# Kernel tuning notes

Hardware: AMD Instinct MI355X
Metric: run time of the kernel (lower is better)

## Reference

```python
import jax, jax.numpy as jnp
import numpy as np

EMBED = 1024
HEADS = 16
HEAD_DIM = EMBED // HEADS
SCALING = HEAD_DIM ** -0.5
R = 16
LORA_SCALE = 32.0 / R  # alpha / r
NEG = jnp.finfo(jnp.float32).min


def lora_linear(x, W, A, B):
    # y = x @ W.T + (x @ A.T) @ B.T * scale   (LinearLora, bias=False)
    return x @ W.T + ((x @ A.T) @ B.T) * LORA_SCALE


def setup_inputs() -> dict:
    key = jax.random.key(0)
    ks = jax.random.split(key, 14)
    B, T, D = 1, 4096, EMBED
    hidden_states = jax.random.normal(ks[0], (B, T, D), jnp.float32)
    # causal additive mask (bsz, 1, tgt, src): 0 on/below diag, dtype-min above
    i = jnp.arange(T)
    causal = jnp.where(i[:, None] >= i[None, :], 0.0, NEG).astype(jnp.float32)
    attention_mask = jnp.broadcast_to(causal, (B, 1, T, T))
    s = 0.02
    def w(k, shape):
        return jax.random.normal(k, shape, jnp.float32) * s
    return dict(
        hidden_states=hidden_states,
        attention_mask=attention_mask,
        Wq=w(ks[1], (D, D)), Wk=w(ks[2], (D, D)), Wv=w(ks[3], (D, D)), Wo=w(ks[4], (D, D)),
        Aq=w(ks[5], (R, D)), Bq=jnp.zeros((D, R), jnp.float32) + w(ks[6], (D, R)),
        Ak=w(ks[7], (R, D)), Bk=w(ks[8], (D, R)),
        Av=w(ks[9], (R, D)), Bv=w(ks[10], (D, R)),
        Ao=w(ks[11], (R, D)), Bo=w(ks[12], (D, R)),
    )


def reference(hidden_states, attention_mask, Wq, Wk, Wv, Wo,
              Aq, Bq, Ak, Bk, Av, Bv, Ao, Bo):
    bsz, tgt_len, _ = hidden_states.shape
    H, Hd = HEADS, HEAD_DIM

    q = lora_linear(hidden_states, Wq, Aq, Bq) * SCALING
    k = lora_linear(hidden_states, Wk, Ak, Bk)
    v = lora_linear(hidden_states, Wv, Av, Bv)

    # (b, t, H, Hd)
    q = q.reshape(bsz, tgt_len, H, Hd)
    k = k.reshape(bsz, tgt_len, H, Hd)
    v = v.reshape(bsz, tgt_len, H, Hd)

    # scores (b, H, t, s)
    attn = jnp.einsum('bthd,bshd->bhts', q, k)
    attn = attn + attention_mask
    attn = jnp.maximum(attn, NEG)
    attn = jax.nn.softmax(attn, axis=-1)  # dropout p=0 / eval mode

    out = jnp.einsum('bhts,bshd->bthd', attn, v)
    out = out.reshape(bsz, tgt_len, H * Hd)
    out = lora_linear(out, Wo, Ao, Bo)
    return out
```

## Files before the change

### kernel.cpp

```cpp
#include <hip/hip_runtime.h>
#include <cmath>
#include <cstdint>

typedef unsigned short u16;
typedef __attribute__((ext_vector_type(8))) __bf16 bf16x8;
typedef __attribute__((ext_vector_type(4))) __bf16 bf16x4;
typedef __attribute__((ext_vector_type(4))) short s16x4;
typedef __attribute__((ext_vector_type(4))) float f32x4;

__device__ __forceinline__ u16 f2bf(float f) {
    union { float f; unsigned u; } v; v.f = f;
    unsigned r = v.u + 0x7fffu + ((v.u >> 16) & 1u);
    return (u16)(r >> 16);
}

__device__ __forceinline__ void gload_lds(const u16* g, u16* l) {
    __builtin_amdgcn_global_load_lds((__attribute__((address_space(1))) void*)g,
                                     (__attribute__((address_space(3))) void*)l,
                                     16, 0, 0);
}

__device__ __forceinline__ f32x4 mfma16(s16x4 a, s16x4 b, f32x4 c) {
#if __has_builtin(__builtin_amdgcn_mfma_f32_16x16x16bf16_1k)
    return __builtin_amdgcn_mfma_f32_16x16x16bf16_1k(a, b, c, 0, 0, 0);
#else
    asm("v_mfma_f32_16x16x16_bf16 %0, %1, %2, %3"
        : "=v"(c) : "v"(a), "v"(b), "0"(c));
    return c;
#endif
}

__global__ __launch_bounds__(256) void prep_all(
        const float* __restrict__ X,
        const float* __restrict__ Wq, const float* __restrict__ Wk,
        const float* __restrict__ Wv, const float* __restrict__ Wo,
        const float* __restrict__ Aq, const float* __restrict__ Bq,
        const float* __restrict__ Ak, const float* __restrict__ Bk,
        const float* __restrict__ Av, const float* __restrict__ Bv,
        const float* __restrict__ Ao, const float* __restrict__ Bo,
        u16* __restrict__ Wqkv, u16* __restrict__ Wob, u16* __restrict__ Xb) {
    const int p = blockIdx.y;
    const int idx = blockIdx.x * 256 + threadIdx.x;
    if (p == 4) {
        float4 v = ((const float4*)X)[idx];
        ushort4 o;
        o.x = f2bf(v.x); o.y = f2bf(v.y); o.z = f2bf(v.z); o.w = f2bf(v.w);
        ((ushort4*)Xb)[idx] = o;
        return;
    }
    const int n = idx >> 10, d = idx & 1023;
    const float* W; const float* A; const float* B;
    switch (p) {
        case 0: W = Wq; A = Aq; B = Bq; break;
        case 1: W = Wk; A = Ak; B = Bk; break;
        case 2: W = Wv; A = Av; B = Bv; break;
        default: W = Wo; A = Ao; B = Bo; break;
    }
    float lora = 0.f;
#pragma unroll
    for (int r = 0; r < 16; r++) lora += B[n * 16 + r] * A[r * 1024 + d];
    float v = W[idx] + 2.0f * lora;
    if (p == 0) v *= 0.125f * 1.44269504088896340736f;
    if (p < 3) Wqkv[(size_t)p * 1048576 + idx] = f2bf(v);
    else       Wob[idx] = f2bf(v);
}

template <bool F32OUT>
__global__ __launch_bounds__(256, 3) void gemm_bt(const u16* __restrict__ A,
                                                  const u16* __restrict__ B,
                                                  void* __restrict__ C, int ldc) {
    __shared__ __align__(16) u16 As[128 * 64];
    __shared__ __align__(16) u16 Bs[128 * 64];
    const int tid = threadIdx.x;
    const int lane = tid & 63, wave = tid >> 6;
    const int quad = lane >> 4, l16 = lane & 15;
    const int wm = (wave >> 1) * 64, wn = (wave & 1) * 64;
    const size_t m0 = (size_t)blockIdx.y * 128, n0 = (size_t)blockIdx.x * 128;
    const u16* Ap = A + m0 * 1024;
    const u16* Bp = B + n0 * 1024;
    const int xsw = l16 & 7;
    f32x4 acc[4][4] = {};
    for (int k0 = 0; k0 < 1024; k0 += 64) {
#pragma unroll
        for (int hh = 0; hh < 4; hh++) {
            int c = tid + hh * 256;
            int row = c >> 3, cg = (c & 7) ^ (row & 7);
            gload_lds(Ap + (size_t)row * 1024 + k0 + cg * 8, As + c * 8);
            gload_lds(Bp + (size_t)row * 1024 + k0 + cg * 8, Bs + c * 8);
        }
        asm volatile("s_waitcnt vmcnt(0)" ::: "memory");
        __syncthreads();
#pragma unroll
        for (int kf = 0; kf < 2; kf++) {
            bf16x8 af[4], bfr[4];
#pragma unroll
            for (int i = 0; i < 4; i++) {
                af[i]  = *(const bf16x8*)(As + (wm + i * 16 + l16) * 64
                                             + ((kf * 4 + quad) ^ xsw) * 8);
                bfr[i] = *(const bf16x8*)(Bs + (wn + i * 16 + l16) * 64
                                             + ((kf * 4 + quad) ^ xsw) * 8);
            }
#pragma unroll
            for (int mi = 0; mi < 4; mi++)
#pragma unroll
                for (int ni = 0; ni < 4; ni++)
                    acc[mi][ni] = __builtin_amdgcn_mfma_f32_16x16x32_bf16(
                            af[mi], bfr[ni], acc[mi][ni], 0, 0, 0);
        }
        __syncthreads();
    }
#pragma unroll
    for (int mi = 0; mi < 4; mi++)
#pragma unroll
        for (int ni = 0; ni < 4; ni++)
#pragma unroll
            for (int r = 0; r < 4; r++) {
                size_t row = m0 + wm + mi * 16 + quad * 4 + r;
                size_t col = n0 + wn + ni * 16 + l16;
                if (F32OUT) ((float*)C)[row * ldc + col] = acc[mi][ni][r];
                else        ((u16*)C)[row * ldc + col] = f2bf(acc[mi][ni][r]);
            }
}

template <bool F32OUT>
__global__ __launch_bounds__(256, 3) void gemm_bt64(const u16* __restrict__ A,
                                                    const u16* __restrict__ B,
                                                    void* __restrict__ C, int ldc) {
    __shared__ __align__(16) u16 As[64 * 64];
    __shared__ __align__(16) u16 Bs[128 * 64];
    const int tid = threadIdx.x;
    const int lane = tid & 63, wave = tid >> 6;
    const int quad = lane >> 4, l16 = lane & 15;
    const int wm = (wave >> 1) * 32, wn = (wave & 1) * 64;
    const size_t m0 = (size_t)blockIdx.y * 64, n0 = (size_t)blockIdx.x * 128;
    const u16* Ap = A + m0 * 1024;
    const u16* Bp = B + n0 * 1024;
    const int xsw = l16 & 7;
    f32x4 acc[2][4] = {};
    for (int k0 = 0; k0 < 1024; k0 += 64) {
#pragma unroll
        for (int hh = 0; hh < 2; hh++) {
            int c = tid + hh * 256;
            int row = c >> 3, cg = (c & 7) ^ (row & 7);
            gload_lds(Ap + (size_t)row * 1024 + k0 + cg * 8, As + c * 8);
        }
#pragma unroll
        for (int hh = 0; hh < 4; hh++) {
            int c = tid + hh * 256;
            int row = c >> 3, cg = (c & 7) ^ (row & 7);
            gload_lds(Bp + (size_t)row * 1024 + k0 + cg * 8, Bs + c * 8);
        }
        asm volatile("s_waitcnt vmcnt(0)" ::: "memory");
        __syncthreads();
#pragma unroll
        for (int kf = 0; kf < 2; kf++) {
            bf16x8 af[2], bfr[4];
#pragma unroll
            for (int i = 0; i < 2; i++)
                af[i] = *(const bf16x8*)(As + (wm + i * 16 + l16) * 64
                                            + ((kf * 4 + quad) ^ xsw) * 8);
#pragma unroll
            for (int i = 0; i < 4; i++)
                bfr[i] = *(const bf16x8*)(Bs + (wn + i * 16 + l16) * 64
                                             + ((kf * 4 + quad) ^ xsw) * 8);
#pragma unroll
            for (int mi = 0; mi < 2; mi++)
#pragma unroll
                for (int ni = 0; ni < 4; ni++)
                    acc[mi][ni] = __builtin_amdgcn_mfma_f32_16x16x32_bf16(
                            af[mi], bfr[ni], acc[mi][ni], 0, 0, 0);
        }
        __syncthreads();
    }
#pragma unroll
    for (int mi = 0; mi < 2; mi++)
#pragma unroll
        for (int ni = 0; ni < 4; ni++)
#pragma unroll
            for (int r = 0; r < 4; r++) {
                size_t row = m0 + wm + mi * 16 + quad * 4 + r;
                size_t col = n0 + wn + ni * 16 + l16;
                if (F32OUT) ((float*)C)[row * ldc + col] = acc[mi][ni][r];
                else        ((u16*)C)[row * ldc + col] = f2bf(acc[mi][ni][r]);
            }
}

__global__ __launch_bounds__(256) void transpose_v(const u16* __restrict__ Y,
                                                   u16* __restrict__ Vt) {
    __shared__ u16 tile[64][68];
    const int dv0 = blockIdx.x * 64;
    const int t0  = blockIdx.y * 64;
    const int tid = threadIdx.x;
#pragma unroll
    for (int p = 0; p < 4; p++) {
        int pos = tid + p * 256;
        int row = pos >> 4;
        int c4  = (pos & 15) * 4;
        ushort4 v = *(const ushort4*)(Y + (size_t)(t0 + row) * 3072 + 2048 + dv0 + c4);
        tile[row][c4 + 0] = v.x; tile[row][c4 + 1] = v.y;
        tile[row][c4 + 2] = v.z; tile[row][c4 + 3] = v.w;
    }
    __syncthreads();
#pragma unroll
    for (int p = 0; p < 4; p++) {
        int pos = tid + p * 256;
        int orow = pos >> 4;
        int oc4  = (pos & 15) * 4;
        ushort4 o;
        o.x = tile[oc4 + 0][orow]; o.y = tile[oc4 + 1][orow];
        o.z = tile[oc4 + 2][orow]; o.w = tile[oc4 + 3][orow];
        *(ushort4*)(Vt + (size_t)(dv0 + orow) * 4096 + t0 + oc4) = o;
    }
}

__device__ const unsigned char SCHED[48] = {
    (1<<6)|31, (0<<6)|15, (1<<6)|30, (2<<6)|30, (2<<6)|29, (0<<6)|14, (2<<6)|28, (1<<6)|27,
    (2<<6)|27, (0<<6)|13, (2<<6)|26, (2<<6)|25, (0<<6)|12, (1<<6)|24, (2<<6)|24, (2<<6)|23,
    (2<<6)|31, (1<<6)|29, (1<<6)|28, (1<<6)|26, (1<<6)|25, (1<<6)|23, (1<<6)|22, (1<<6)|21,
    (1<<6)|20, (2<<6)|20, (1<<6)|19, (2<<6)|19, (2<<6)|21, (2<<6)|22, (0<<6)|10, (0<<6)|11,
    (0<<6)|0,  (0<<6)|1,  (0<<6)|2,  (0<<6)|3,  (0<<6)|4,  (0<<6)|5,  (0<<6)|6,  (0<<6)|7,
    (1<<6)|16, (2<<6)|16, (1<<6)|18, (0<<6)|9,  (1<<6)|17, (2<<6)|17, (2<<6)|18, (0<<6)|8
};

__global__ __launch_bounds__(256, 3) void flash_attn(
        const u16* __restrict__ Y,
        const u16* __restrict__ Vt,
        u16* __restrict__ O,
        float* __restrict__ OpA,
        float* __restrict__ OpB,
        float* __restrict__ lA,
        float* __restrict__ lB) {
    __shared__ __align__(16) u16 lds[24576];
    const int tid = threadIdx.x;
    const int wave = tid >> 6, lane = tid & 63;
    const int quad = lane >> 4, l16 = lane & 15;
    const int bid = blockIdx.x;
    const int g = bid >> 4, h = bid & 15;
    const int sc = SCHED[g];
    const int p = sc & 63, mode = sc >> 6;
    const int t0 = (mode == 2) ? p + 1 : 0;
    const int t1 = (mode == 1) ? p + 1 : 2 * p + 2;
    const int q0w = p * 128 + wave * 32;
    const u16* Kbase = Y + 1024 + h * 64;
    const u16* Vbase = Vt + (size_t)(h * 64) * 4096;
    const int xsw = l16 & 7;

#define STAGE(TT, BUF) do {                                                   \
        const int sss = (TT) * 64;                                            \
        u16* Kn_ = (BUF);                                                     \
        _Pragma("unroll")                                                     \
        for (int pp = 0; pp < 2; pp++) {                                      \
            int c = pp * 256 + tid;                                           \
            int row_ = c >> 3, cg_ = (c & 7) ^ (row_ & 7);                    \
            gload_lds(Kbase + (size_t)(sss + row_) * 3072 + cg_ * 8,          \
                      Kn_ + c * 8);                                           \
            gload_lds(Vbase + (size_t)row_ * 4096 + sss + cg_ * 8,            \
                      Kn_ + 4096 + c * 8);                                    \
        }                                                                     \
    } while (0)

    bf16x8 qf[2][2];
#pragma unroll
    for (int qh = 0; qh < 2; qh++)
#pragma unroll
        for (int kf = 0; kf < 2; kf++)
            qf[qh][kf] = *(const bf16x8*)(Y + (size_t)(q0w + qh * 16 + l16) * 3072
                                            + h * 64 + kf * 32 + quad * 8);

    f32x4 oaccT[2][4] = {};
    f32x4 lacc[2] = {};
    const s16x4 ones = { (short)0x3F80, (short)0x3F80,
                         (short)0x3F80, (short)0x3F80 };

    STAGE(t0, lds);
    if (t0 + 1 < t1) STAGE(t0 + 1, lds + 8192);

    int cur = 0;
    int nxt = 2;
#pragma unroll 1
    for (int t = t0; t < t1; t++) {
        const int s0 = t * 64;
        u16* Ks = lds + cur * 8192;
        u16* Vs = Ks + 4096;
        if (t + 1 < t1) asm volatile("s_waitcnt vmcnt(4)" ::: "memory");
        else            asm volatile("s_waitcnt vmcnt(0)" ::: "memory");
        __syncthreads();

        if (t + 2 < t1) STAGE(t + 2, lds + nxt * 8192);

        bf16x8 kfr[4][2];
#pragma unroll
        for (int ni = 0; ni < 4; ni++) {
            int row = ni * 16 + l16;
            kfr[ni][0] = *(const bf16x8*)(Ks + row * 64 + ((quad) ^ xsw) * 8);
            kfr[ni][1] = *(const bf16x8*)(Ks + row * 64 + ((4 + quad) ^ xsw) * 8);
        }
        s16x4 vfr[4][4];
#pragma unroll
        for (int nj = 0; nj < 4; nj++) {
            int row = nj * 16 + l16;
#pragma unroll
            for (int ni = 0; ni < 4; ni++) {
                int cc = ni * 2 + (quad >> 1);
                vfr[nj][ni] = *(const s16x4*)(Vs + row * 64 + (cc ^ xsw) * 8
                                                 + (quad & 1) * 4);
            }
        }

        const bool diag = (t >= 2 * p);
#pragma unroll
        for (int qh = 0; qh < 2; qh++) {
            f32x4 sacc[4] = {};
            __builtin_amdgcn_s_setprio(1);
#pragma unroll
            for (int ni = 0; ni < 4; ni++) {
                sacc[ni] = __builtin_amdgcn_mfma_f32_16x16x32_bf16(
                        kfr[ni][0], qf[qh][0], sacc[ni], 0, 0, 0);
                sacc[ni] = __builtin_amdgcn_mfma_f32_16x16x32_bf16(
                        kfr[ni][1], qf[qh][1], sacc[ni], 0, 0, 0);
            }
            __builtin_amdgcn_s_setprio(0);
            const int qg = q0w + qh * 16 + l16;
#pragma unroll
            for (int ni = 0; ni < 4; ni++) {
                if (diag) {
#pragma unroll
                    for (int r = 0; r < 4; r++) {
                        int sg = s0 + ni * 16 + quad * 4 + r;
                        if (sg > qg) sacc[ni][r] = -INFINITY;
                    }
                }
                f32x4 pe;
#pragma unroll
                for (int r = 0; r < 4; r++)
                    pe[r] = __builtin_amdgcn_exp2f(sacc[ni][r]);
                bf16x4 tt = { (__bf16)pe[0], (__bf16)pe[1],
                              (__bf16)pe[2], (__bf16)pe[3] };
                s16x4 pf = __builtin_bit_cast(s16x4, tt);
                __builtin_amdgcn_s_setprio(1);
                lacc[qh] = mfma16(ones, pf, lacc[qh]);
#pragma unroll
                for (int nj = 0; nj < 4; nj++)
                    oaccT[qh][nj] = mfma16(vfr[nj][ni], pf, oaccT[qh][nj]);
                __builtin_amdgcn_s_setprio(0);
            }
        }
        cur = (cur == 2) ? 0 : cur + 1;
        nxt = (nxt == 2) ? 0 : nxt + 1;
    }
#undef STAGE

    __syncthreads();
    if (mode == 0) {
        u16* scr = lds + wave * 1152;
#pragma unroll
        for (int qh = 0; qh < 2; qh++) {
            float inv = 1.0f / lacc[qh][0];
#pragma unroll
            for (int nj = 0; nj < 4; nj++) {
                bf16x4 t4 = { (__bf16)(oaccT[qh][nj][0] * inv),
                              (__bf16)(oaccT[qh][nj][1] * inv),
                              (__bf16)(oaccT[qh][nj][2] * inv),
                              (__bf16)(oaccT[qh][nj][3] * inv) };
                *(s16x4*)(scr + l16 * 72 + nj * 16 + quad * 4) =
                        __builtin_bit_cast(s16x4, t4);
            }
            asm volatile("s_waitcnt lgkmcnt(0)" ::: "memory");
#pragma unroll
            for (int pp = 0; pp < 2; pp++) {
                int row = pp * 8 + (lane >> 3);
                int seg = (lane & 7) * 8;
                bf16x8 d = *(const bf16x8*)(scr + row * 72 + seg);
                *(bf16x8*)(O + (size_t)(q0w + qh * 16 + row) * 1024 + h * 64 + seg) = d;
            }
            asm volatile("s_waitcnt lgkmcnt(0)" ::: "memory");
        }
    } else {
        float* Op = (mode == 1) ? OpA : OpB;
        float* lp = (mode == 1) ? lA : lB;
        float* scr = (float*)lds + wave * 1088;
#pragma unroll
        for (int qh = 0; qh < 2; qh++) {
#pragma unroll
            for (int nj = 0; nj < 4; nj++)
                *(f32x4*)(scr + l16 * 68 + nj * 16 + quad * 4) = oaccT[qh][nj];
            asm volatile("s_waitcnt lgkmcnt(0)" ::: "memory");
#pragma unroll
            for (int it = 0; it < 4; it++) {
                int row = (lane >> 4) + it * 4;
                int seg = (lane & 15) * 4;
                f32x4 d = *(const f32x4*)(scr + row * 68 + seg);
                *(f32x4*)(Op + (size_t)(q0w + qh * 16 + row - 2048) * 1024
                             + h * 64 + seg) = d;
            }
            if (lane < 16)
                lp[(size_t)(q0w + qh * 16 + lane - 2048) * 16 + h] = lacc[qh][0];
            asm volatile("s_waitcnt lgkmcnt(0)" ::: "memory");
        }
    }
}

__global__ __launch_bounds__(256) void combine_o(
        const float* __restrict__ OpA, const float* __restrict__ OpB,
        const float* __restrict__ lA, const float* __restrict__ lB,
        u16* __restrict__ O) {
    const int idx = blockIdx.x * 256 + threadIdx.x;
    const int r = idx >> 7;
    const int c8 = (idx & 127) * 8;
    const int h = c8 >> 6;
    const float inv = 1.0f / (lA[r * 16 + h] + lB[r * 16 + h]);
    const float* a = OpA + (size_t)r * 1024 + c8;
    const float* b = OpB + (size_t)r * 1024 + c8;
    float4 a0 = *(const float4*)a, a1 = *(const float4*)(a + 4);
    float4 b0 = *(const float4*)b, b1 = *(const float4*)(b + 4);
    ushort4 o0, o1;
    o0.x = f2bf((a0.x + b0.x) * inv); o0.y = f2bf((a0.y + b0.y) * inv);
    o0.z = f2bf((a0.z + b0.z) * inv); o0.w = f2bf((a0.w + b0.w) * inv);
    o1.x = f2bf((a1.x + b1.x) * inv); o1.y = f2bf((a1.y + b1.y) * inv);
    o1.z = f2bf((a1.z + b1.z) * inv); o1.w = f2bf((a1.w + b1.w) * inv);
    u16* op = O + (size_t)(2048 + r) * 1024 + c8;
    *(ushort4*)op = o0;
    *(ushort4*)(op + 4) = o1;
}


extern "C" void kernel_launch(void* const* d_in, const int* in_sizes, int n_in,
                              void* d_out, int out_size, void* d_ws, size_t ws_size,
                              hipStream_t stream) {
    const float* X  = (const float*)d_in[0];
    const float* Wq = (const float*)d_in[2];
    const float* Wk = (const float*)d_in[3];
    const float* Wv = (const float*)d_in[4];
    const float* Wo = (const float*)d_in[5];
    const float* Aq = (const float*)d_in[6];
    const float* Bq = (const float*)d_in[7];
    const float* Ak = (const float*)d_in[8];
    const float* Bk = (const float*)d_in[9];
    const float* Av = (const float*)d_in[10];
    const float* Bv = (const float*)d_in[11];
    const float* Ao = (const float*)d_in[12];
    const float* Bo = (const float*)d_in[13];

    char* ws = (char*)d_ws;
    u16*   Xb   = (u16*)(ws);
    float* OpA  = (float*)(ws);
    u16*   Wqkv = (u16*)(ws + (8u  << 20));
    float* OpB  = (float*)(ws + (8u  << 20));
    u16*   Y    = (u16*)(ws + (16u << 20));
    u16*   Vt   = (u16*)(ws + (40u << 20));
    u16*   Ob   = (u16*)(ws + (48u << 20));
    u16*   Wob  = (u16*)(ws + (56u << 20));
    float* lA   = (float*)(ws + (58u << 20));
    float* lB   = (float*)(ws + (58u << 20) + (128u << 10));

    prep_all<<<dim3(4096, 5), 256, 0, stream>>>(X, Wq, Wk, Wv, Wo, Aq, Bq, Ak, Bk,
                                                Av, Bv, Ao, Bo, Wqkv, Wob, Xb);
    gemm_bt<false><<<dim3(24, 32), 256, 0, stream>>>(Xb, Wqkv, Y, 3072);
    transpose_v<<<dim3(16, 64), 256, 0, stream>>>(Y, Vt);
    flash_attn<<<dim3(768), 256, 0, stream>>>(Y, Vt, Ob, OpA, OpB, lA, lB);
    combine_o<<<dim3(1024), 256, 0, stream>>>(OpA, OpB, lA, lB, Ob);
    gemm_bt64<true><<<dim3(8, 64), 256, 0, stream>>>(Ob, Wob, d_out, 1024);
}
```

Baseline: 255.9 us.

## Replace QKV GEMM with 256x192 double-buffered tile kernel using 512 threads

```diff
diff --git a/kernel.cpp b/kernel.cpp
--- a/kernel.cpp
+++ b/kernel.cpp
@@ -65,60 +65,98 @@
     else       Wob[idx] = f2bf(v);
 }
 
-template <bool F32OUT>
-__global__ __launch_bounds__(256, 3) void gemm_bt(const u16* __restrict__ A,
-                                                  const u16* __restrict__ B,
-                                                  void* __restrict__ C, int ldc) {
-    __shared__ __align__(16) u16 As[128 * 64];
-    __shared__ __align__(16) u16 Bs[128 * 64];
+__global__ __launch_bounds__(512, 2) void gemm_bt256(const u16* __restrict__ A,
+                                                     const u16* __restrict__ B,
+                                                     u16* __restrict__ C, int ldc) {
+    __shared__ __align__(16) u16 As[2][256 * 64];
+    __shared__ __align__(16) u16 Bs[2][192 * 64];
     const int tid = threadIdx.x;
-    const int lane = tid & 63, wave = tid >> 6;
+    const int lane = tid & 63;
+    const int wave = tid >> 6;
     const int quad = lane >> 4, l16 = lane & 15;
-    const int wm = (wave >> 1) * 64, wn = (wave & 1) * 64;
-    const size_t m0 = (size_t)blockIdx.y * 128, n0 = (size_t)blockIdx.x * 128;
+    const int wm = (wave >> 2) * 128;
+    const int wn = (wave & 3) * 48;
+    const size_t m0 = (size_t)blockIdx.y * 256, n0 = (size_t)blockIdx.x * 192;
     const u16* Ap = A + m0 * 1024;
     const u16* Bp = B + n0 * 1024;
     const int xsw = l16 & 7;
-    f32x4 acc[4][4] = {};
-    for (int k0 = 0; k0 < 1024; k0 += 64) {
-#pragma unroll
-        for (int hh = 0; hh < 4; hh++) {
-            int c = tid + hh * 256;
-            int row = c >> 3, cg = (c & 7) ^ (row & 7);
-            gload_lds(Ap + (size_t)row * 1024 + k0 + cg * 8, As + c * 8);
-            gload_lds(Bp + (size_t)row * 1024 + k0 + cg * 8, Bs + c * 8);
-        }
-        asm volatile("s_waitcnt vmcnt(0)" ::: "memory");
+
+#define STAGEA(T, BUF) do {                                                   \
+        _Pragma("unroll")                                                     \
+        for (int hh = 0; hh < 4; hh++) {                                      \
+            int c = tid + hh * 512;                                           \
+            int row_ = c >> 3, cg_ = (c & 7) ^ (row_ & 7);                    \
+            gload_lds(Ap + (size_t)row_ * 1024 + (T) * 64 + cg_ * 8,          \
+                      (BUF) + c * 8);                                         \
+        }                                                                     \
+    } while (0)
+#define STAGEB(T, BUF) do {                                                   \
+        _Pragma("unroll")                                                     \
+        for (int hh = 0; hh < 3; hh++) {                                      \
+            int c = tid + hh * 512;                                           \
+            int row_ = c >> 3, cg_ = (c & 7) ^ (row_ & 7);                    \
+            gload_lds(Bp + (size_t)row_ * 1024 + (T) * 64 + cg_ * 8,          \
+                      (BUF) + c * 8);                                         \
+        }                                                                     \
+    } while (0)
+
+    f32x4 acc[8][3] = {};
+
+    STAGEA(0, As[0]);
+    STAGEB(0, Bs[0]);
+    asm volatile("s_waitcnt vmcnt(0)" ::: "memory");
+    __syncthreads();
+
+#pragma unroll 1
+    for (int t = 0; t < 16; t++) {
+        const u16* Asc = As[t & 1];
+        const u16* Bsc = Bs[t & 1];
+        if (t + 1 < 16) {
+            STAGEA(t + 1, As[(t + 1) & 1]);
+            STAGEB(t + 1, Bs[(t + 1) & 1]);
+        }
+        bf16x8 bfr[3][2];
+#pragma unroll
+        for (int nj = 0; nj < 3; nj++)
+#pragma unroll
+            for (int kf = 0; kf < 2; kf++)
+                bfr[nj][kf] = *(const bf16x8*)(Bsc + (wn + nj * 16 + l16) * 64
+                                                   + ((kf * 4 + quad) ^ xsw) * 8);
+#pragma unroll
+        for (int mh = 0; mh < 2; mh++) {
+            bf16x8 af[4][2];
+#pragma unroll
+            for (int mi = 0; mi < 4; mi++)
+#pragma unroll
+                for (int kf = 0; kf < 2; kf++)
+                    af[mi][kf] = *(const bf16x8*)(Asc + (wm + mh * 64 + mi * 16 + l16) * 64
+                                                      + ((kf * 4 + quad) ^ xsw) * 8);
+            __builtin_amdgcn_s_setprio(1);
+#pragma unroll
+            for (int kf = 0; kf < 2; kf++)
+#pragma unroll
+                for (int mi = 0; mi < 4; mi++)
+#pragma unroll
+                    for (int nj = 0; nj < 3; nj++)
+                        acc[mh * 4 + mi][nj] = __builtin_amdgcn_mfma_f32_16x16x32_bf16(
+                                af[mi][kf], bfr[nj][kf], acc[mh * 4 + mi][nj], 0, 0, 0);
+            __builtin_amdgcn_s_setprio(0);
+        }
+        if (t + 1 < 16) asm volatile("s_waitcnt vmcnt(0)" ::: "memory");
         __syncthreads();
-#pragma unroll
-        for (int kf = 0; kf < 2; kf++) {
-            bf16x8 af[4], bfr[4];
-#pragma unroll
-            for (int i = 0; i < 4; i++) {
-                af[i]  = *(const bf16x8*)(As + (wm + i * 16 + l16) * 64
-                                             + ((kf * 4 + quad) ^ xsw) * 8);
-                bfr[i] = *(const bf16x8*)(Bs + (wn + i * 16 + l16) * 64
-                                             + ((kf * 4 + quad) ^ xsw) * 8);
-            }
-#pragma unroll
-            for (int mi = 0; mi < 4; mi++)
-#pragma unroll
-                for (int ni = 0; ni < 4; ni++)
-                    acc[mi][ni] = __builtin_amdgcn_mfma_f32_16x16x32_bf16(
-                            af[mi], bfr[ni], acc[mi][ni], 0, 0, 0);
-        }
-        __syncthreads();
-    }
-#pragma unroll
-    for (int mi = 0; mi < 4; mi++)
-#pragma unroll
-        for (int ni = 0; ni < 4; ni++)
+    }
+#undef STAGEA
+#undef STAGEB
+
+#pragma unroll
+    for (int mi = 0; mi < 8; mi++)
+#pragma unroll
+        for (int nj = 0; nj < 3; nj++)
 #pragma unroll
             for (int r = 0; r < 4; r++) {
                 size_t row = m0 + wm + mi * 16 + quad * 4 + r;
-                size_t col = n0 + wn + ni * 16 + l16;
-                if (F32OUT) ((float*)C)[row * ldc + col] = acc[mi][ni][r];
-                else        ((u16*)C)[row * ldc + col] = f2bf(acc[mi][ni][r]);
+                size_t col = n0 + wn + nj * 16 + l16;
+                C[row * ldc + col] = f2bf(acc[mi][nj][r]);
             }
 }
 
@@ -455,7 +493,7 @@
 
     prep_all<<<dim3(4096, 5), 256, 0, stream>>>(X, Wq, Wk, Wv, Wo, Aq, Bq, Ak, Bk,
                                                 Av, Bv, Ao, Bo, Wqkv, Wob, Xb);
-    gemm_bt<false><<<dim3(24, 32), 256, 0, stream>>>(Xb, Wqkv, Y, 3072);
+    gemm_bt256<<<dim3(16, 16), 512, 0, stream>>>(Xb, Wqkv, Y, 3072);
     transpose_v<<<dim3(16, 64), 256, 0, stream>>>(Y, Vt);
     flash_attn<<<dim3(768), 256, 0, stream>>>(Y, Vt, Ob, OpA, OpB, lA, lB);
     combine_o<<<dim3(1024), 256, 0, stream>>>(OpA, OpB, lA, lB, Ob);
```

New measurement: 261.4 us. 2.1% more time.
